# Performance work log

Hardware: AMD Instinct MI355X
Metric: run time of the kernel (lower is better)

The kernel has to match this reference:

```python
import jax, jax.numpy as jnp
import numpy as np

D_MODEL = 1024
D_FF = 4096
N_HEADS = 16
D_K = D_MODEL // N_HEADS
EPS = 1e-6
NEG_INF = 1.0e9


def _layer_norm(x, g, b):
    mu = jnp.mean(x, axis=-1, keepdims=True)
    var = jnp.mean(jnp.square(x - mu), axis=-1, keepdims=True)
    return (x - mu) / jnp.sqrt(var + EPS) * g + b


def setup_inputs() -> dict:
    key = jax.random.key(0)
    ks = jax.random.split(key, 16)
    s = 1.0 / np.sqrt(D_MODEL)
    inp = {
        'x': jax.random.normal(ks[0], (4, 2048, D_MODEL), dtype=jnp.float32),
        'e_mask': jnp.ones((4, 1, 2048), dtype=jnp.int32),
        'ln1_g': jnp.ones((D_MODEL,), jnp.float32),
        'ln1_b': jnp.zeros((D_MODEL,), jnp.float32),
        'wq': jax.random.normal(ks[1], (D_MODEL, D_MODEL), jnp.float32) * s,
        'bq': jnp.zeros((D_MODEL,), jnp.float32),
        'wk': jax.random.normal(ks[2], (D_MODEL, D_MODEL), jnp.float32) * s,
        'bk': jnp.zeros((D_MODEL,), jnp.float32),
        'wv': jax.random.normal(ks[3], (D_MODEL, D_MODEL), jnp.float32) * s,
        'bv': jnp.zeros((D_MODEL,), jnp.float32),
        'w0': jax.random.normal(ks[4], (D_MODEL, D_MODEL), jnp.float32) * s,
        'b0': jnp.zeros((D_MODEL,), jnp.float32),
        'ln2_g': jnp.ones((D_MODEL,), jnp.float32),
        'ln2_b': jnp.zeros((D_MODEL,), jnp.float32),
        'w1': jax.random.normal(ks[5], (D_MODEL, D_FF), jnp.float32) * s,
        'b1': jnp.zeros((D_FF,), jnp.float32),
        'w2': jax.random.normal(ks[6], (D_FF, D_MODEL), jnp.float32) * (1.0 / np.sqrt(D_FF)),
        'b2': jnp.zeros((D_MODEL,), jnp.float32),
    }
    return inp


def reference(x, e_mask, ln1_g, ln1_b, wq, bq, wk, bk, wv, bv, w0, b0,
              ln2_g, ln2_b, w1, b1, w2, b2):
    B, S, _ = x.shape
    # --- pre-LN multihead attention (dropout = identity in eval) ---
    x1 = _layer_norm(x, ln1_g, ln1_b)
    q = (x1 @ wq + bq).reshape(B, S, N_HEADS, D_K).transpose(0, 2, 1, 3)
    k = (x1 @ wk + bk).reshape(B, S, N_HEADS, D_K).transpose(0, 2, 1, 3)
    v = (x1 @ wv + bv).reshape(B, S, N_HEADS, D_K).transpose(0, 2, 1, 3)
    scores = jnp.einsum('bhqd,bhkd->bhqk', q, k) / np.sqrt(D_K).astype(np.float32)
    mask = e_mask[:, None, :, :]  # [B,1,1,S] broadcast over heads and queries
    scores = jnp.where(mask == 0, -NEG_INF, scores)
    attn = jax.nn.softmax(scores, axis=-1)
    ctx = jnp.einsum('bhqk,bhkd->bhqd', attn, v)
    ctx = ctx.transpose(0, 2, 1, 3).reshape(B, S, D_MODEL)
    x = x + (ctx @ w0 + b0)
    # --- pre-LN feed-forward ---
    x2 = _layer_norm(x, ln2_g, ln2_b)
    h = jax.nn.relu(x2 @ w1 + b1)
    x = x + (h @ w2 + b2)
    return x
```

## Files before the change

### kernel.cpp

```cpp
#include <hip/hip_runtime.h>
#include <cstdint>
#include <cstddef>

typedef __bf16 bf16;
typedef __bf16 bf16x8 __attribute__((ext_vector_type(8)));
typedef __bf16 bf16x4 __attribute__((ext_vector_type(4)));
typedef float  f32x4  __attribute__((ext_vector_type(4)));
typedef float  f32x16 __attribute__((ext_vector_type(16)));

#define D_MODEL 1024
#define D_FF    4096
#define SEQ     2048
#define NB      4
#define NH      16
#define DKH     64
#define MTOT    (NB * SEQ)

__device__ __forceinline__ void gl_lds16(const void* g, void* l) {
  __builtin_amdgcn_global_load_lds(
      (__attribute__((address_space(1))) unsigned int*)(void*)g,
      (__attribute__((address_space(3))) unsigned int*)l, 16, 0, 0);
}

#define SWZ(row, kb) (((row) << 7) + ((kb) ^ (((row) & 7) << 4)))

__device__ __forceinline__ unsigned cvtpk(float lo, float hi_) {
  unsigned r;
  asm("v_cvt_pk_bf16_f32 %0, %1, %2" : "=v"(r) : "v"(lo), "v"(hi_));
  return r;
}
__device__ __forceinline__ void pl32swap(unsigned& a, unsigned& b) {
  asm volatile("v_permlane32_swap_b32 %0, %1" : "+v"(a), "+v"(b));
}

__global__ __launch_bounds__(256) void k_transp(const float* __restrict__ W,
                                                bf16* __restrict__ Wt, int R, int C) {
  __shared__ float tile[32][33];
  const int c0 = blockIdx.x * 32, r0 = blockIdx.y * 32;
  const int t = threadIdx.x;
  const int rl = t >> 5, cl = t & 31;
#pragma unroll
  for (int i = 0; i < 4; ++i)
    tile[rl + i * 8][cl] = W[(size_t)(r0 + rl + i * 8) * C + c0 + cl];
  __syncthreads();
#pragma unroll
  for (int i = 0; i < 4; ++i)
    Wt[(size_t)(c0 + rl + i * 8) * R + r0 + cl] = (bf16)tile[cl][rl + i * 8];
}

__global__ __launch_bounds__(256) void k_ln(const float* __restrict__ x,
                                            const float* __restrict__ g,
                                            const float* __restrict__ b,
                                            bf16* __restrict__ out) {
  const int row = blockIdx.x;
  const int t = threadIdx.x;
  const float4 v = ((const float4*)(x + (size_t)row * D_MODEL))[t];
  float s  = v.x + v.y + v.z + v.w;
  float s2 = v.x * v.x + v.y * v.y + v.z * v.z + v.w * v.w;
#pragma unroll
  for (int off = 1; off < 64; off <<= 1) {
    s  += __shfl_xor(s, off);
    s2 += __shfl_xor(s2, off);
  }
  __shared__ float red[8];
  const int wv = t >> 6;
  if ((t & 63) == 0) { red[wv] = s; red[4 + wv] = s2; }
  __syncthreads();
  s  = red[0] + red[1] + red[2] + red[3];
  s2 = red[4] + red[5] + red[6] + red[7];
  const float mu   = s * (1.f / D_MODEL);
  const float var  = s2 * (1.f / D_MODEL) - mu * mu;
  const float rstd = rsqrtf(var + 1e-6f);
  const float4 gv = ((const float4*)g)[t];
  const float4 bv = ((const float4*)b)[t];
  bf16x4 o;
  o[0] = (bf16)((v.x - mu) * rstd * gv.x + bv.x);
  o[1] = (bf16)((v.y - mu) * rstd * gv.y + bv.y);
  o[2] = (bf16)((v.z - mu) * rstd * gv.z + bv.z);
  o[3] = (bf16)((v.w - mu) * rstd * gv.w + bv.w);
  *(bf16x4*)(out + (size_t)row * D_MODEL + t * 4) = o;
}

template <int EPI>
__global__ __launch_bounds__(256) void k_gemm(
    const bf16* __restrict__ A, const bf16* __restrict__ Bt,
    const float* __restrict__ bias, const float* __restrict__ biasK,
    const float* __restrict__ biasV, float alpha,
    bf16* __restrict__ obf, float* __restrict__ of32,
    const float* __restrict__ resid,
    int M, int N, int K) {
  __shared__ bf16 As[128 * 32];
  __shared__ bf16 Bs[128 * 32];
  const int t = threadIdx.x, lane = t & 63, w = t >> 6;
  const int wr = w >> 1, wc = w & 1;
  const int tm = blockIdx.y * 128, tn = blockIdx.x * 128;

  f32x4 acc[4][4] = {};

  const int arow = w * 32 + (lane >> 2);
  const int acol = (lane & 3) * 8;
  const bf16* aS0 = A  + (size_t)(tm + arow) * K + acol;
  const bf16* aS1 = aS0 + (size_t)16 * K;
  const bf16* bS0 = Bt + (size_t)(tn + arow) * K + acol;
  const bf16* bS1 = bS0 + (size_t)16 * K;
  bf16* aD0 = (bf16*)As + w * 1024;
  bf16* aD1 = aD0 + 512;
  bf16* bD0 = (bf16*)Bs + w * 1024;
  bf16* bD1 = bD0 + 512;

  const bf16* aRd[4];
  const bf16* bRd[4];
#pragma unroll
  for (int m = 0; m < 4; ++m)
    aRd[m] = As + (wr * 64 + m * 16 + (lane & 15)) * 32 + (lane >> 4) * 8;
#pragma unroll
  for (int n = 0; n < 4; ++n)
    bRd[n] = Bs + (wc * 64 + n * 16 + (lane & 15)) * 32 + (lane >> 4) * 8;

  for (int k0 = 0; k0 < K; k0 += 32) {
    __syncthreads();
    gl_lds16(aS0 + k0, aD0);
    gl_lds16(aS1 + k0, aD1);
    gl_lds16(bS0 + k0, bD0);
    gl_lds16(bS1 + k0, bD1);
    __syncthreads();
    bf16x8 af[4], bfr[4];
#pragma unroll
    for (int m = 0; m < 4; ++m) af[m] = *(const bf16x8*)aRd[m];
#pragma unroll
    for (int n = 0; n < 4; ++n) bfr[n] = *(const bf16x8*)bRd[n];
#pragma unroll
    for (int m = 0; m < 4; ++m)
#pragma unroll
      for (int n = 0; n < 4; ++n)
        acc[m][n] = __builtin_amdgcn_mfma_f32_16x16x32_bf16(af[m], bfr[n], acc[m][n], 0, 0, 0);
  }

  const int row0 = tm + wr * 64 + (lane >> 4) * 4;
  const int col0 = tn + wc * 64 + (lane & 15);
  const int which = tn >> 10;
  const float* bp = (EPI == 1) ? (which == 0 ? bias : (which == 1 ? biasK : biasV)) : bias;
  const float af_ = (EPI == 1) ? (which == 0 ? alpha : 1.f) : alpha;
  bf16* qkvB = (EPI == 1) ? obf + (size_t)which * MTOT * D_MODEL : obf;
#pragma unroll
  for (int n = 0; n < 4; ++n) {
    const int col = col0 + n * 16;
    const float bv = (EPI == 1) ? bp[col & 1023] : bp[col];
#pragma unroll
    for (int m = 0; m < 4; ++m) {
#pragma unroll
      for (int r = 0; r < 4; ++r) {
        const int row = row0 + m * 16 + r;
        float val = acc[m][n][r] + bv;
        if constexpr (EPI == 1) {
          const int bb = row >> 11, ss = row & 2047, hh = (col >> 6) & 15, dd = col & 63;
          qkvB[(((size_t)bb * NH + hh) * SEQ + ss) * DKH + dd] = (bf16)(val * af_);
        } else if constexpr (EPI == 2) {
          const size_t idx = (size_t)row * N + col;
          of32[idx] = resid[idx] + val;
        } else {
          obf[(size_t)row * N + col] = (bf16)fmaxf(val, 0.f);
        }
      }
    }
  }
}

__global__ __launch_bounds__(512, 4) void k_attn(
    const bf16* __restrict__ q, const bf16* __restrict__ k, const bf16* __restrict__ v,
    const int* __restrict__ emask, bf16* __restrict__ ctx) {
  __shared__ bf16 Kl[64 * 64];
  __shared__ bf16 Vt[64 * 64];
  __shared__ float Msk[64];
  __shared__ int MskFlag;
  const int t = threadIdx.x, lane = t & 63, w = t >> 6;
  const int hi = lane >> 5;
  const int l31 = lane & 31;
  const unsigned swz = (lane & 7) << 4;
  const int bh = blockIdx.x, b = bh >> 4, h = bh & 15;
  const int q0 = blockIdx.y * 256;
  const bf16* qp = q + (size_t)bh * SEQ * DKH;
  const bf16* kp = k + (size_t)bh * SEQ * DKH;
  const bf16* vp = v + (size_t)bh * SEQ * DKH;
  const int* mp = emask + b * SEQ;

  const int qrow = q0 + w * 32 + l31;
  const bf16* qpr = qp + (size_t)qrow * DKH + hi * 8;
  bf16x8 qf[4];
#pragma unroll
  for (int ks = 0; ks < 4; ++ks) qf[ks] = *(const bf16x8*)(qpr + ks * 16);

  const int krow = w * 8 + (lane >> 3);
  const int kcolE = (((lane & 7) * 16) ^ ((lane >> 3) << 4)) >> 1;
  const bf16* kSrc = kp + (size_t)krow * DKH + kcolE;
  char* kDst = (char*)Kl + w * 1024;

  const int vKey = t >> 3, vD0 = (t & 7) * 8;
  const bf16* vSrc = vp + (size_t)vKey * DKH + vD0;

  f32x16 O0 = {}, O1 = {};
  float mrun = -3e38f, lrun = 0.f;

  for (int kt = 0; kt < SEQ; kt += 64) {
    __syncthreads();
    gl_lds16(kSrc + (size_t)kt * DKH, kDst);
    const bf16x8 vv = *(const bf16x8*)(vSrc + (size_t)kt * DKH);
#pragma unroll
    for (int j = 0; j < 8; ++j)
      *(bf16*)((char*)Vt + ((vD0 + j) << 7) + ((vKey * 2) ^ (j << 4))) = vv[j];
    if (t < 64) {
      const float mv = (mp[kt + t] == 0) ? -1e9f : 0.f;
      Msk[t] = mv;
      const unsigned long long bal = __ballot(mv != 0.f);
      if (t == 0) MskFlag = (bal != 0ull);
    }
    __syncthreads();

    f32x16 s0 = {}, s1 = {};
#pragma unroll
    for (int ks = 0; ks < 4; ++ks) {
      const bf16x8 kf = *(const bf16x8*)((const char*)Kl + (l31 << 7) + ((ks * 32 + hi * 16) ^ swz));
      s0 = __builtin_amdgcn_mfma_f32_32x32x16_bf16(kf, qf[ks], s0, 0, 0, 0);
    }
#pragma unroll
    for (int ks = 0; ks < 4; ++ks) {
      const bf16x8 kf = *(const bf16x8*)((const char*)Kl + ((32 + l31) << 7) + ((ks * 32 + hi * 16) ^ swz));
      s1 = __builtin_amdgcn_mfma_f32_32x32x16_bf16(kf, qf[ks], s1, 0, 0, 0);
    }
    if (MskFlag) {
#pragma unroll
      for (int g = 0; g < 4; ++g)
#pragma unroll
        for (int j = 0; j < 4; ++j) {
          s0[g * 4 + j] += Msk[g * 8 + hi * 4 + j];
          s1[g * 4 + j] += Msk[32 + g * 8 + hi * 4 + j];
        }
    }

    float mx = s0[0];
#pragma unroll
    for (int r = 1; r < 16; ++r) mx = fmaxf(mx, s0[r]);
#pragma unroll
    for (int r = 0; r < 16; ++r) mx = fmaxf(mx, s1[r]);
    mx = fmaxf(mx, __shfl_xor(mx, 32));
    const float mnew = fmaxf(mrun, mx);
    const float scal = exp2f(mrun - mnew);
    mrun = mnew;
    float ts = 0.f;
#pragma unroll
    for (int r = 0; r < 16; ++r) { const float p = exp2f(s0[r] - mnew); s0[r] = p; ts += p; }
#pragma unroll
    for (int r = 0; r < 16; ++r) { const float p = exp2f(s1[r] - mnew); s1[r] = p; ts += p; }
    ts += __shfl_xor(ts, 32);
    lrun = lrun * scal + ts;
#pragma unroll
    for (int r = 0; r < 16; ++r) { O0[r] *= scal; O1[r] *= scal; }

#define PVSTEP(S, bsel, ks)                                                          \
    {                                                                                \
      unsigned c0 = cvtpk(S[8 * bsel + 0], S[8 * bsel + 1]);                         \
      unsigned c1 = cvtpk(S[8 * bsel + 2], S[8 * bsel + 3]);                         \
      unsigned c2 = cvtpk(S[8 * bsel + 4], S[8 * bsel + 5]);                         \
      unsigned c3 = cvtpk(S[8 * bsel + 6], S[8 * bsel + 7]);                         \
      pl32swap(c0, c2);                                                              \
      pl32swap(c1, c3);                                                              \
      union { unsigned u[4]; bf16x8 vv_; } pu = {{c0, c1, c2, c3}};                  \
      const bf16x8 vf0 = *(const bf16x8*)((const char*)Vt + (l31 << 7) + (((ks) * 32 + hi * 16) ^ swz)); \
      O0 = __builtin_amdgcn_mfma_f32_32x32x16_bf16(vf0, pu.vv_, O0, 0, 0, 0);        \
      const bf16x8 vf1 = *(const bf16x8*)((const char*)Vt + ((32 + l31) << 7) + (((ks) * 32 + hi * 16) ^ swz)); \
      O1 = __builtin_amdgcn_mfma_f32_32x32x16_bf16(vf1, pu.vv_, O1, 0, 0, 0);        \
    }
    PVSTEP(s0, 0, 0)
    PVSTEP(s0, 1, 1)
    PVSTEP(s1, 0, 2)
    PVSTEP(s1, 1, 3)
#undef PVSTEP
  }

  const float rl = 1.f / lrun;
  bf16* cp = ctx + ((size_t)b * SEQ + qrow) * D_MODEL + h * 64;
#pragma unroll
  for (int r = 0; r < 16; ++r) {
    const int d0 = (r & 3) + 8 * (r >> 2) + hi * 4;
    cp[d0]      = (bf16)(O0[r] * rl);
    cp[32 + d0] = (bf16)(O1[r] * rl);
  }
}

extern "C" void kernel_launch(void* const* d_in, const int* in_sizes, int n_in,
                              void* d_out, int out_size, void* d_ws, size_t ws_size,
                              hipStream_t stream) {
  (void)in_sizes; (void)n_in; (void)out_size; (void)ws_size;
  const float* x    = (const float*)d_in[0];
  const int*   em   = (const int*)d_in[1];
  const float* ln1g = (const float*)d_in[2];
  const float* ln1b = (const float*)d_in[3];
  const float* wq   = (const float*)d_in[4];
  const float* bq   = (const float*)d_in[5];
  const float* wk   = (const float*)d_in[6];
  const float* bk   = (const float*)d_in[7];
  const float* wv   = (const float*)d_in[8];
  const float* bv   = (const float*)d_in[9];
  const float* w0   = (const float*)d_in[10];
  const float* b0   = (const float*)d_in[11];
  const float* ln2g = (const float*)d_in[12];
  const float* ln2b = (const float*)d_in[13];
  const float* w1   = (const float*)d_in[14];
  const float* b1   = (const float*)d_in[15];
  const float* w2   = (const float*)d_in[16];
  const float* b2   = (const float*)d_in[17];
  float* out = (float*)d_out;

  char* ws = (char*)d_ws;
  const size_t MB = 1u << 20;
  bf16* wqT = (bf16*)(ws + 0 * MB);
  bf16* wkT = (bf16*)(ws + 2 * MB);
  bf16* wvT = (bf16*)(ws + 4 * MB);
  bf16* w0T = (bf16*)(ws + 6 * MB);
  bf16* w1T = (bf16*)(ws + 8 * MB);
  bf16* w2T = (bf16*)(ws + 16 * MB);
  bf16* x1  = (bf16*)(ws + 24 * MB);
  bf16* qB  = (bf16*)(ws + 40 * MB);
  bf16* kB  = (bf16*)(ws + 56 * MB);
  bf16* vB  = (bf16*)(ws + 72 * MB);
  bf16* cB  = (bf16*)(ws + 88 * MB);
  bf16* hB  = (bf16*)(ws + 40 * MB);

  k_transp<<<dim3(32, 32),  256, 0, stream>>>(wq, wqT, 1024, 1024);
  k_transp<<<dim3(32, 32),  256, 0, stream>>>(wk, wkT, 1024, 1024);
  k_transp<<<dim3(32, 32),  256, 0, stream>>>(wv, wvT, 1024, 1024);
  k_transp<<<dim3(32, 32),  256, 0, stream>>>(w0, w0T, 1024, 1024);
  k_transp<<<dim3(128, 32), 256, 0, stream>>>(w1, w1T, 1024, 4096);
  k_transp<<<dim3(32, 128), 256, 0, stream>>>(w2, w2T, 4096, 1024);

  k_ln<<<MTOT, 256, 0, stream>>>(x, ln1g, ln1b, x1);

  k_gemm<1><<<dim3(24, MTOT / 128), 256, 0, stream>>>(
      x1, wqT, bq, bk, bv, 0.125f * 1.44269504f, qB, nullptr, nullptr, MTOT, 3072, 1024);

  k_attn<<<dim3(64, 8), 512, 0, stream>>>(qB, kB, vB, em, cB);

  const dim3 g1024(8, MTOT / 128);
  k_gemm<2><<<g1024, 256, 0, stream>>>(cB, w0T, b0, nullptr, nullptr, 1.0f, nullptr, out, x, MTOT, 1024, 1024);

  k_ln<<<MTOT, 256, 0, stream>>>(out, ln2g, ln2b, x1);

  k_gemm<3><<<dim3(32, MTOT / 128), 256, 0, stream>>>(x1, w1T, b1, nullptr, nullptr, 1.0f, hB, nullptr, nullptr, MTOT, 4096, 1024);

  k_gemm<2><<<g1024, 256, 0, stream>>>(hB, w2T, b2, nullptr, nullptr, 1.0f, nullptr, out, out, MTOT, 1024, 4096);
}
```

Measured before the change: 639.4 us.

## Rebuild GEMM as double-buffered 256x128 pipeline; add lazy softmax rescale

The GEMM now uses 512-thread blocks with 256x128 tiles and BK=64, double-buffered swizzled LDS, and global-to-LDS prefetch interleaved with MFMA groups under s_setprio. Block IDs are remapped so that neighbouring tiles are spread across XCDs. The aim is to hide the load latency of the old single-buffered loop, which synchronised twice per K step. Attention gets a new V transpose-load pattern and skips the online-softmax rescale unless the running max grows by more than a threshold. The three QKV weight transposes now land contiguously in one buffer. Risks are much higher LDS and register use, which limits occupancy, and bf16 accuracy, since unnormalised probabilities can reach 256.

Measured after the change: 545.7 us. 1.17x faster.

```diff
diff --git a/kernel.cpp b/kernel.cpp
--- a/kernel.cpp
+++ b/kernel.cpp
@@ -21,8 +21,6 @@
       (__attribute__((address_space(1))) unsigned int*)(void*)g,
       (__attribute__((address_space(3))) unsigned int*)l, 16, 0, 0);
 }
-
-#define SWZ(row, kb) (((row) << 7) + ((kb) ^ (((row) & 7) << 4)))
 
 __device__ __forceinline__ unsigned cvtpk(float lo, float hi_) {
   unsigned r;
@@ -82,62 +80,106 @@
 }
 
 template <int EPI>
-__global__ __launch_bounds__(256) void k_gemm(
+__global__ __launch_bounds__(512, 2) void k_gemm(
     const bf16* __restrict__ A, const bf16* __restrict__ Bt,
     const float* __restrict__ bias, const float* __restrict__ biasK,
     const float* __restrict__ biasV, float alpha,
     bf16* __restrict__ obf, float* __restrict__ of32,
     const float* __restrict__ resid,
     int M, int N, int K) {
-  __shared__ bf16 As[128 * 32];
-  __shared__ bf16 Bs[128 * 32];
+  __shared__ char lds[2][49152];
   const int t = threadIdx.x, lane = t & 63, w = t >> 6;
-  const int wr = w >> 1, wc = w & 1;
-  const int tm = blockIdx.y * 128, tn = blockIdx.x * 128;
+  const int wm = w >> 1, wn = w & 1;
+
+  const int gx = gridDim.x;
+  const int nwg = gx * gridDim.y;
+  int id = blockIdx.x + blockIdx.y * gx;
+  id = (id & 7) * (nwg >> 3) + (id >> 3);
+  const int tn = (id % gx) * 128;
+  const int tm = (id / gx) * 256;
+
+  const int srow = w * 16 + (lane >> 3);
+  const int scol = 8 * ((lane & 7) ^ (lane >> 3));
+  const bf16* aS = A  + (size_t)(tm + srow) * K + scol;
+  const bf16* bS = Bt + (size_t)(tn + srow) * K + scol;
+  const int dstOff = w * 2048;
+
+  const int rA = (wm * 64 + (lane & 15)) * 128;
+  const int rB = 32768 + (wn * 64 + (lane & 15)) * 128;
+  const int cS0 = (((lane >> 4) * 16)      ) ^ ((lane & 7) << 4);
+  const int cS1 = (64 + ((lane >> 4) * 16) ) ^ ((lane & 7) << 4);
 
   f32x4 acc[4][4] = {};
-
-  const int arow = w * 32 + (lane >> 2);
-  const int acol = (lane & 3) * 8;
-  const bf16* aS0 = A  + (size_t)(tm + arow) * K + acol;
-  const bf16* aS1 = aS0 + (size_t)16 * K;
-  const bf16* bS0 = Bt + (size_t)(tn + arow) * K + acol;
-  const bf16* bS1 = bS0 + (size_t)16 * K;
-  bf16* aD0 = (bf16*)As + w * 1024;
-  bf16* aD1 = aD0 + 512;
-  bf16* bD0 = (bf16*)Bs + w * 1024;
-  bf16* bD1 = bD0 + 512;
-
-  const bf16* aRd[4];
-  const bf16* bRd[4];
-#pragma unroll
-  for (int m = 0; m < 4; ++m)
-    aRd[m] = As + (wr * 64 + m * 16 + (lane & 15)) * 32 + (lane >> 4) * 8;
-#pragma unroll
-  for (int n = 0; n < 4; ++n)
-    bRd[n] = Bs + (wc * 64 + n * 16 + (lane & 15)) * 32 + (lane >> 4) * 8;
-
-  for (int k0 = 0; k0 < K; k0 += 32) {
-    __syncthreads();
-    gl_lds16(aS0 + k0, aD0);
-    gl_lds16(aS1 + k0, aD1);
-    gl_lds16(bS0 + k0, bD0);
-    gl_lds16(bS1 + k0, bD1);
-    __syncthreads();
-    bf16x8 af[4], bfr[4];
-#pragma unroll
-    for (int m = 0; m < 4; ++m) af[m] = *(const bf16x8*)aRd[m];
-#pragma unroll
-    for (int n = 0; n < 4; ++n) bfr[n] = *(const bf16x8*)bRd[n];
-#pragma unroll
-    for (int m = 0; m < 4; ++m)
-#pragma unroll
-      for (int n = 0; n < 4; ++n)
-        acc[m][n] = __builtin_amdgcn_mfma_f32_16x16x32_bf16(af[m], bfr[n], acc[m][n], 0, 0, 0);
-  }
-
-  const int row0 = tm + wr * 64 + (lane >> 4) * 4;
-  const int col0 = tn + wc * 64 + (lane & 15);
+  const int KT = K >> 6;
+
+  gl_lds16(aS,                 lds[0] + dstOff);
+  gl_lds16(aS + 8 * K,         lds[0] + dstOff + 1024);
+  gl_lds16(aS + 128 * K,       lds[0] + 16384 + dstOff);
+  gl_lds16(aS + 136 * K,       lds[0] + 16384 + dstOff + 1024);
+  gl_lds16(bS,                 lds[0] + 32768 + dstOff);
+  gl_lds16(bS + 8 * K,         lds[0] + 32768 + dstOff + 1024);
+  gl_lds16(aS + 64,            lds[1] + dstOff);
+  gl_lds16(aS + 8 * K + 64,    lds[1] + dstOff + 1024);
+  asm volatile("s_waitcnt vmcnt(2)" ::: "memory");
+  __builtin_amdgcn_s_barrier();
+  __builtin_amdgcn_sched_barrier(0);
+
+#define RD(buf, off) (*(const bf16x8*)((buf) + (off)))
+#define MM(m, n, s) acc[m][n] = __builtin_amdgcn_mfma_f32_16x16x32_bf16(a[m][s], b[n][s], acc[m][n], 0, 0, 0)
+
+  for (int tt = 0; tt < KT; ++tt) {
+    char* bufc = lds[tt & 1];
+    char* bufn = lds[(tt & 1) ^ 1];
+    const int k1 = (tt + 1 < KT ? tt + 1 : KT - 1) * 64;
+    const int k2 = (tt + 2 < KT ? tt + 2 : KT - 1) * 64;
+    bf16x8 a[4][2], b[4][2];
+    a[0][0] = RD(bufc, rA + cS0);          a[0][1] = RD(bufc, rA + cS1);
+    a[1][0] = RD(bufc, rA + 2048 + cS0);   a[1][1] = RD(bufc, rA + 2048 + cS1);
+    b[0][0] = RD(bufc, rB + cS0);
+    b[1][0] = RD(bufc, rB + 2048 + cS0);
+    b[2][0] = RD(bufc, rB + 4096 + cS0);
+    b[3][0] = RD(bufc, rB + 6144 + cS0);
+    gl_lds16(aS + 128 * K + k1, bufn + 16384 + dstOff);
+    gl_lds16(aS + 136 * K + k1, bufn + 16384 + dstOff + 1024);
+    __builtin_amdgcn_s_setprio(1);
+    MM(0,0,0); MM(0,1,0); MM(0,2,0); MM(0,3,0);
+    MM(1,0,0); MM(1,1,0); MM(1,2,0); MM(1,3,0);
+    __builtin_amdgcn_s_setprio(0);
+    a[2][0] = RD(bufc, rA + 4096 + cS0);   a[2][1] = RD(bufc, rA + 4096 + cS1);
+    a[3][0] = RD(bufc, rA + 6144 + cS0);   a[3][1] = RD(bufc, rA + 6144 + cS1);
+    b[0][1] = RD(bufc, rB + cS1);
+    b[1][1] = RD(bufc, rB + 2048 + cS1);
+    b[2][1] = RD(bufc, rB + 4096 + cS1);
+    b[3][1] = RD(bufc, rB + 6144 + cS1);
+    gl_lds16(bS + k1,         bufn + 32768 + dstOff);
+    gl_lds16(bS + 8 * K + k1, bufn + 32768 + dstOff + 1024);
+    __builtin_amdgcn_s_setprio(1);
+    MM(2,0,0); MM(2,1,0); MM(2,2,0); MM(2,3,0);
+    MM(3,0,0); MM(3,1,0); MM(3,2,0); MM(3,3,0);
+    __builtin_amdgcn_s_setprio(0);
+    asm volatile("s_waitcnt lgkmcnt(0)" ::: "memory");
+    __builtin_amdgcn_s_barrier();
+    __builtin_amdgcn_sched_barrier(0);
+    gl_lds16(aS + k2,         bufc + dstOff);
+    gl_lds16(aS + 8 * K + k2, bufc + dstOff + 1024);
+    __builtin_amdgcn_s_setprio(1);
+    MM(0,0,1); MM(0,1,1); MM(0,2,1); MM(0,3,1);
+    MM(1,0,1); MM(1,1,1); MM(1,2,1); MM(1,3,1);
+    __builtin_amdgcn_s_setprio(0);
+    __builtin_amdgcn_s_setprio(1);
+    MM(2,0,1); MM(2,1,1); MM(2,2,1); MM(2,3,1);
+    MM(3,0,1); MM(3,1,1); MM(3,2,1); MM(3,3,1);
+    __builtin_amdgcn_s_setprio(0);
+    asm volatile("s_waitcnt vmcnt(2)" ::: "memory");
+    __builtin_amdgcn_s_barrier();
+    __builtin_amdgcn_sched_barrier(0);
+  }
+#undef RD
+#undef MM
+  asm volatile("s_waitcnt vmcnt(0)" ::: "memory");
+
+  const int row0 = tm + wm * 64 + (lane >> 4) * 4;
+  const int col0 = tn + wn * 64 + (lane & 15);
   const int which = tn >> 10;
   const float* bp = (EPI == 1) ? (which == 0 ? bias : (which == 1 ? biasK : biasV)) : bias;
   const float af_ = (EPI == 1) ? (which == 0 ? alpha : 1.f) : alpha;
@@ -195,8 +237,8 @@
   const bf16* kSrc = kp + (size_t)krow * DKH + kcolE;
   char* kDst = (char*)Kl + w * 1024;
 
-  const int vKey = t >> 3, vD0 = (t & 7) * 8;
-  const bf16* vSrc = vp + (size_t)vKey * DKH + vD0;
+  const ushort* vU = (const ushort*)vp;
+  bf16* vDst = (bf16*)((char*)Vt + (lane << 7) + ((w * 16) ^ ((lane & 7) << 4)));
 
   f32x16 O0 = {}, O1 = {};
   float mrun = -3e38f, lrun = 0.f;
@@ -204,10 +246,11 @@
   for (int kt = 0; kt < SEQ; kt += 64) {
     __syncthreads();
     gl_lds16(kSrc + (size_t)kt * DKH, kDst);
-    const bf16x8 vv = *(const bf16x8*)(vSrc + (size_t)kt * DKH);
+    union { ushort u[8]; bf16x8 v8; } vb;
 #pragma unroll
     for (int j = 0; j < 8; ++j)
-      *(bf16*)((char*)Vt + ((vD0 + j) << 7) + ((vKey * 2) ^ (j << 4))) = vv[j];
+      vb.u[j] = vU[(size_t)(kt + w * 8 + j) * 64 + lane];
+    *(bf16x8*)vDst = vb.v8;
     if (t < 64) {
       const float mv = (mp[kt + t] == 0) ? -1e9f : 0.f;
       Msk[t] = mv;
@@ -243,18 +286,21 @@
 #pragma unroll
     for (int r = 0; r < 16; ++r) mx = fmaxf(mx, s1[r]);
     mx = fmaxf(mx, __shfl_xor(mx, 32));
-    const float mnew = fmaxf(mrun, mx);
-    const float scal = exp2f(mrun - mnew);
-    mrun = mnew;
+    if (!__all((int)(mx - mrun <= 8.f))) {
+      const float mnew = fmaxf(mrun, mx);
+      const float scal = exp2f(mrun - mnew);
+      mrun = mnew;
+      lrun *= scal;
+#pragma unroll
+      for (int r = 0; r < 16; ++r) { O0[r] *= scal; O1[r] *= scal; }
+    }
     float ts = 0.f;
 #pragma unroll
-    for (int r = 0; r < 16; ++r) { const float p = exp2f(s0[r] - mnew); s0[r] = p; ts += p; }
-#pragma unroll
-    for (int r = 0; r < 16; ++r) { const float p = exp2f(s1[r] - mnew); s1[r] = p; ts += p; }
+    for (int r = 0; r < 16; ++r) { const float p = exp2f(s0[r] - mrun); s0[r] = p; ts += p; }
+#pragma unroll
+    for (int r = 0; r < 16; ++r) { const float p = exp2f(s1[r] - mrun); s1[r] = p; ts += p; }
     ts += __shfl_xor(ts, 32);
-    lrun = lrun * scal + ts;
-#pragma unroll
-    for (int r = 0; r < 16; ++r) { O0[r] *= scal; O1[r] *= scal; }
+    lrun += ts;
 
 #define PVSTEP(S, bsel, ks)                                                          \
     {                                                                                \
@@ -314,8 +360,6 @@
   char* ws = (char*)d_ws;
   const size_t MB = 1u << 20;
   bf16* wqT = (bf16*)(ws + 0 * MB);
-  bf16* wkT = (bf16*)(ws + 2 * MB);
-  bf16* wvT = (bf16*)(ws + 4 * MB);
   bf16* w0T = (bf16*)(ws + 6 * MB);
   bf16* w1T = (bf16*)(ws + 8 * MB);
   bf16* w2T = (bf16*)(ws + 16 * MB);
@@ -326,26 +370,26 @@
   bf16* cB  = (bf16*)(ws + 88 * MB);
   bf16* hB  = (bf16*)(ws + 40 * MB);
 
-  k_transp<<<dim3(32, 32),  256, 0, stream>>>(wq, wqT, 1024, 1024);
-  k_transp<<<dim3(32, 32),  256, 0, stream>>>(wk, wkT, 1024, 1024);
-  k_transp<<<dim3(32, 32),  256, 0, stream>>>(wv, wvT, 1024, 1024);
+  k_transp<<<dim3(32, 32),  256, 0, stream>>>(wq, wqT,                   1024, 1024);
+  k_transp<<<dim3(32, 32),  256, 0, stream>>>(wk, wqT + 1024 * 1024,     1024, 1024);
+  k_transp<<<dim3(32, 32),  256, 0, stream>>>(wv, wqT + 2 * 1024 * 1024, 1024, 1024);
   k_transp<<<dim3(32, 32),  256, 0, stream>>>(w0, w0T, 1024, 1024);
   k_transp<<<dim3(128, 32), 256, 0, stream>>>(w1, w1T, 1024, 4096);
   k_transp<<<dim3(32, 128), 256, 0, stream>>>(w2, w2T, 4096, 1024);
 
   k_ln<<<MTOT, 256, 0, stream>>>(x, ln1g, ln1b, x1);
 
-  k_gemm<1><<<dim3(24, MTOT / 128), 256, 0, stream>>>(
+  k_gemm<1><<<dim3(24, MTOT / 256), 512, 0, stream>>>(
       x1, wqT, bq, bk, bv, 0.125f * 1.44269504f, qB, nullptr, nullptr, MTOT, 3072, 1024);
 
   k_attn<<<dim3(64, 8), 512, 0, stream>>>(qB, kB, vB, em, cB);
 
-  const dim3 g1024(8, MTOT / 128);
-  k_gemm<2><<<g1024, 256, 0, stream>>>(cB, w0T, b0, nullptr, nullptr, 1.0f, nullptr, out, x, MTOT, 1024, 1024);
+  const dim3 g1024(8, MTOT / 256);
+  k_gemm<2><<<g1024, 512, 0, stream>>>(cB, w0T, b0, nullptr, nullptr, 1.0f, nullptr, out, x, MTOT, 1024, 1024);
 
   k_ln<<<MTOT, 256, 0, stream>>>(out, ln2g, ln2b, x1);
 
-  k_gemm<3><<<dim3(32, MTOT / 128), 256, 0, stream>>>(x1, w1T, b1, nullptr, nullptr, 1.0f, hB, nullptr, nullptr, MTOT, 4096, 1024);
-
-  k_gemm<2><<<g1024, 256, 0, stream>>>(hB, w2T, b2, nullptr, nullptr, 1.0f, nullptr, out, out, MTOT, 1024, 4096);
-}
+  k_gemm<3><<<dim3(32, MTOT / 256), 512, 0, stream>>>(x1, w1T, b1, nullptr, nullptr, 1.0f, hB, nullptr, nullptr, MTOT, 4096, 1024);
+
+  k_gemm<2><<<g1024, 512, 0, stream>>>(hB, w2T, b2, nullptr, nullptr, 1.0f, nullptr, out, out, MTOT, 1024, 4096);
+}
```
